# Kernel optimization log

Measured on AMD Instinct MI355X. Metric: run time of the kernel, lower is better.

The kernel has to match this reference:

```python
import jax, jax.numpy as jnp
import numpy as np

D_MODEL = 1024
NUM_HEADS = 16
HEAD_DIM = D_MODEL // NUM_HEADS  # used only for score scaling, as in the torch code


def setup_inputs() -> dict:
    key = jax.random.key(0)
    ks = jax.random.split(key, 8)
    B, S, D = 4, 2048, D_MODEL
    w_scale = 1.0 / np.sqrt(D)
    return {
        "x": jax.random.normal(ks[0], (B, S, D), dtype=jnp.float32),
        "Wq": jax.random.normal(ks[1], (D, D), dtype=jnp.float32) * w_scale,
        "bq": jnp.zeros((D,), dtype=jnp.float32),
        "Wk": jax.random.normal(ks[2], (D, D), dtype=jnp.float32) * w_scale,
        "bk": jnp.zeros((D,), dtype=jnp.float32),
        "Wv": jax.random.normal(ks[3], (D, D), dtype=jnp.float32) * w_scale,
        "bv": jnp.zeros((D,), dtype=jnp.float32),
        "temperature_scale": jnp.ones((1,), dtype=jnp.float32),
    }


def reference(x, Wq, bq, Wk, bk, Wv, bv, temperature_scale):
    # q, k, v: (B, S, D) -- no head split in the original module
    q = x @ Wq + bq
    k = x @ Wk + bk
    v = x @ Wv + bv
    scale = jnp.asarray(HEAD_DIM, x.dtype) ** 0.5
    # scores: (B, S, S)
    scores = jnp.einsum("bqd,bkd->bqk", q, k) / scale / temperature_scale[0]
    probs = jax.nn.softmax(scores, axis=-1)
    # per-row attention entropy (B, S, 1)
    entropy = -jnp.sum(probs * jnp.log(probs + 1e-8), axis=-1, keepdims=True)
    attention_output = jnp.einsum("bqk,bkd->bqd", probs, v)
    return attention_output, entropy.mean()
```

## Files before the change

kernel.cpp:

```cpp
#include <hip/hip_runtime.h>
#include <hip/hip_bf16.h>
#include <cstdint>
#include <cstddef>


typedef __attribute__((ext_vector_type(8))) short short8;
typedef __attribute__((ext_vector_type(4))) short short4v;
typedef __attribute__((ext_vector_type(4))) float f32x4;

#define GLOBAL_AS __attribute__((address_space(1)))
#define LDS_AS __attribute__((address_space(3)))

__device__ __forceinline__ void async_load16(const void* g, void* lds) {
  __builtin_amdgcn_global_load_lds((GLOBAL_AS void*)g, (LDS_AS void*)lds, 16, 0, 0);
}

__device__ __forceinline__ short f2bf_s(float x) {
  __hip_bfloat16 h = __float2bfloat16(x);
  return *reinterpret_cast<short*>(&h);
}

template <int MODE>
__device__ __forceinline__
void gemm_body(const __hip_bfloat16* __restrict__ A,
               const __hip_bfloat16* __restrict__ Bt,
               void* __restrict__ Cout,
               const float* __restrict__ bias,
               int K, int lda, int ldb, int ldc,
               __hip_bfloat16* __restrict__ sA,
               __hip_bfloat16* __restrict__ sB,
               int m0, int n0,
               const float* __restrict__ aux,
               float* __restrict__ stats) {
  const int tid  = threadIdx.x;
  const int lane = tid & 63;
  const int wid  = tid >> 6;
  const int wm = (wid >> 1) * 64;
  const int wn = (wid & 1) * 64;
  const int quad = lane >> 4;
  const int rc   = lane & 15;

  f32x4 acc[4][4] = {};

  const int srow = tid >> 3;
  const int scol = ((tid & 7) ^ ((tid >> 3) & 7)) * 8;
  const __hip_bfloat16* Ag = A  + (size_t)(m0 + srow) * lda + scol;
  const __hip_bfloat16* Bg = Bt + (size_t)(n0 + srow) * ldb + scol;

  for (int k0 = 0; k0 < K; k0 += 64) {
#pragma unroll
    for (int p = 0; p < 4; ++p) {
      async_load16(Ag + k0 + (size_t)(32 * p) * lda, &sA[(wid * 64 + 256 * p) * 8]);
      async_load16(Bg + k0 + (size_t)(32 * p) * ldb, &sB[(wid * 64 + 256 * p) * 8]);
    }
    __syncthreads();

#pragma unroll
    for (int kk = 0; kk < 2; ++kk) {
      const int xo = ((kk * 4 + quad) ^ (rc & 7)) * 8;
      short8 af[4], bf[4];
#pragma unroll
      for (int i = 0; i < 4; ++i)
        af[i] = *(const short8*)&sA[(wm + i * 16 + rc) * 64 + xo];
#pragma unroll
      for (int i = 0; i < 4; ++i)
        bf[i] = *(const short8*)&sB[(wn + i * 16 + rc) * 64 + xo];

#pragma unroll
      for (int mi = 0; mi < 4; ++mi)
#pragma unroll
        for (int ni = 0; ni < 4; ++ni)
          acc[mi][ni] = __builtin_amdgcn_mfma_f32_16x16x32_bf16(
              af[mi], bf[ni], acc[mi][ni], 0, 0, 0);
    }
    __syncthreads();
  }

  if (MODE == 3) {
    const int chunk = (n0 + wn) >> 6;
#pragma unroll
    for (int mi = 0; mi < 4; ++mi) {
      float l_acc[4] = {}, w_acc[4] = {};
#pragma unroll
      for (int ni = 0; ni < 4; ++ni)
#pragma unroll
        for (int r = 0; r < 4; ++r) {
          const float xv = acc[mi][ni][r];
          const float e = __expf(xv);
          acc[mi][ni][r] = e;
          l_acc[r] += e;
          w_acc[r] += e * xv;
        }
#pragma unroll
      for (int r = 0; r < 4; ++r) {
        float l = l_acc[r], w = w_acc[r];
#pragma unroll
        for (int off = 1; off < 16; off <<= 1) {
          l += __shfl_xor(l, off);
          w += __shfl_xor(w, off);
        }
        if (rc == 0) {
          const int row = m0 + wm + mi * 16 + quad * 4 + r;
          *(float2*)&stats[((size_t)row * 32 + chunk) * 2] = make_float2(l, w);
        }
      }
#pragma unroll
      for (int ni = 0; ni < 4; ++ni) {
        const int col = n0 + wn + ni * 16 + rc;
#pragma unroll
        for (int r = 0; r < 4; ++r) {
          const int row = m0 + wm + mi * 16 + quad * 4 + r;
          ((__hip_bfloat16*)Cout)[(size_t)row * ldc + col] =
              __float2bfloat16(acc[mi][ni][r]);
        }
      }
    }
  } else if (MODE == 4) {
    float* lred = (float*)sA;
    {
      const int row2 = tid >> 1;
      const float* sp = aux + (size_t)(m0 + row2) * 64 + (tid & 1) * 32;
      float l = 0.f, w = 0.f;
#pragma unroll
      for (int j = 0; j < 8; ++j) {
        const float4 a = *(const float4*)(sp + j * 4);
        l += a.x + a.z;
        w += a.y + a.w;
      }
      l += __shfl_xor(l, 1);
      w += __shfl_xor(w, 1);
      if ((tid & 1) == 0) {
        lred[row2] = 1.0f / l;
        if (stats) stats[m0 + row2] = __logf(l) - w / l;
      }
    }
    __syncthreads();
#pragma unroll
    for (int mi = 0; mi < 4; ++mi) {
      float sc[4];
#pragma unroll
      for (int r = 0; r < 4; ++r)
        sc[r] = lred[wm + mi * 16 + quad * 4 + r];
#pragma unroll
      for (int ni = 0; ni < 4; ++ni) {
        const int col = n0 + wn + ni * 16 + rc;
#pragma unroll
        for (int r = 0; r < 4; ++r) {
          const int row = m0 + wm + mi * 16 + quad * 4 + r;
          ((float*)Cout)[(size_t)row * ldc + col] = acc[mi][ni][r] * sc[r];
        }
      }
    }
  } else {
    const float qsc = (MODE == 1 && aux) ? 1.0f / (8.0f * aux[0]) : 1.0f;
#pragma unroll
    for (int mi = 0; mi < 4; ++mi) {
#pragma unroll
      for (int ni = 0; ni < 4; ++ni) {
        const int col = n0 + wn + ni * 16 + rc;
        const float badd = bias[col];
        if (MODE == 2) {
          const int rowb = m0 + wm + mi * 16 + quad * 4;
          short4v o;
#pragma unroll
          for (int r = 0; r < 4; ++r) o[r] = f2bf_s(acc[mi][ni][r] + badd);
          const size_t idx = (size_t)(rowb >> 11) * (1024u * 2048u) +
                             (size_t)col * 2048u + (size_t)(rowb & 2047);
          *(short4v*)((short*)Cout + idx) = o;
        } else {
#pragma unroll
          for (int r = 0; r < 4; ++r) {
            const int row = m0 + wm + mi * 16 + quad * 4 + r;
            ((__hip_bfloat16*)Cout)[(size_t)row * ldc + col] =
                __float2bfloat16((acc[mi][ni][r] + badd) * qsc);
          }
        }
      }
    }
  }
}


__global__ __launch_bounds__(256)
void qkv_fused(const __hip_bfloat16* __restrict__ xb,
               const __hip_bfloat16* __restrict__ Wt,
               __hip_bfloat16* __restrict__ qb, __hip_bfloat16* __restrict__ kb,
               __hip_bfloat16* __restrict__ vt,
               const float* __restrict__ bq, const float* __restrict__ bk,
               const float* __restrict__ bv, const float* __restrict__ tptr) {
  __shared__ __align__(16) __hip_bfloat16 sA[128 * 64];
  __shared__ __align__(16) __hip_bfloat16 sB[128 * 64];
  const int lin = blockIdx.x;
  const int j = lin & 7, t = lin >> 3;
  const int x = t & 7;
  const int G = j + 8 * (t >> 3);
  const int z = G >> 6, y = G & 63;
  const int m0 = y * 128, n0 = x * 128;

  const __hip_bfloat16* B = Wt + (size_t)z * 1024 * 1024;
  if (z == 0)
    gemm_body<1>(xb, B, qb, bq, 1024, 1024, 1024, 1024, sA, sB, m0, n0, tptr, nullptr);
  else if (z == 1)
    gemm_body<1>(xb, B, kb, bk, 1024, 1024, 1024, 1024, sA, sB, m0, n0, nullptr, nullptr);
  else
    gemm_body<2>(xb, B, vt, bv, 1024, 1024, 1024, 0, sA, sB, m0, n0, nullptr, nullptr);
}

__global__ __launch_bounds__(256)
void scores_swz(const __hip_bfloat16* __restrict__ qb,
                const __hip_bfloat16* __restrict__ kb,
                __hip_bfloat16* __restrict__ Pt,
                float* __restrict__ stats) {
  __shared__ __align__(16) __hip_bfloat16 sA[128 * 64];
  __shared__ __align__(16) __hip_bfloat16 sB[128 * 64];
  const int lin = blockIdx.x;
  const int j = lin & 7, t = lin >> 3;
  const int w = t & 15;
  const int G = j + 8 * (t >> 4);
  const size_t z = G >> 4;
  const int r = G & 15;
  const int y = (r >> 2) * 4 + (w >> 2);
  const int x = (r & 3) * 4 + (w & 3);
  gemm_body<3>(qb + z * 2048 * 1024, kb + z * 2048 * 1024,
               Pt + z * 2048 * 2048, nullptr, 1024, 1024, 1024, 2048,
               sA, sB, y * 128, x * 128, nullptr, stats + z * 2048 * 64);
}

__global__ __launch_bounds__(256)
void pv_swz(const __hip_bfloat16* __restrict__ Pt,
            const __hip_bfloat16* __restrict__ vt,
            float* __restrict__ out,
            const float* __restrict__ stats,
            float* __restrict__ Hrow) {
  __shared__ __align__(16) __hip_bfloat16 sA[128 * 64];
  __shared__ __align__(16) __hip_bfloat16 sB[128 * 64];
  const int lin = blockIdx.x;
  const int j = lin & 7, t = lin >> 3;
  const int w = t & 3;
  const int G = j + 8 * (t >> 2);
  const size_t z = G >> 5;
  const int r = G & 31;
  const int y = (r >> 2) * 2 + (w >> 1);
  const int x = (r & 3) * 2 + (w & 1);
  gemm_body<4>(Pt + z * 2048 * 2048, vt + z * 1024 * 2048,
               out + z * 2048 * 1024, nullptr, 2048, 2048, 2048, 1024,
               sA, sB, y * 128, x * 128,
               stats + z * 2048 * 64,
               (x == 0) ? (Hrow + z * 2048) : nullptr);
}

__global__ __launch_bounds__(256)
void prep_fused(const float* __restrict__ x, __hip_bfloat16* __restrict__ xb,
                const float* __restrict__ Wq, const float* __restrict__ Wk,
                const float* __restrict__ Wv, __hip_bfloat16* __restrict__ Wt) {
  if (blockIdx.x < 4096) {
    const int i = (blockIdx.x * 256 + threadIdx.x) * 8;
    const float4 a = *(const float4*)(x + i);
    const float4 b = *(const float4*)(x + i + 4);
    short8 o;
    o[0] = f2bf_s(a.x); o[1] = f2bf_s(a.y); o[2] = f2bf_s(a.z); o[3] = f2bf_s(a.w);
    o[4] = f2bf_s(b.x); o[5] = f2bf_s(b.y); o[6] = f2bf_s(b.z); o[7] = f2bf_s(b.w);
    *(short8*)((short*)xb + i) = o;
  } else {
    __shared__ float tile[64][65];
    const int b = blockIdx.x - 4096;
    const int z = b >> 8;
    const int rem = b & 255;
    const int c0 = (rem & 15) * 64;
    const int r0 = (rem >> 4) * 64;
    const float* src = (z == 0) ? Wq : (z == 1) ? Wk : Wv;
    __hip_bfloat16* dst = Wt + (size_t)z * 1024 * 1024;
    const int lane = threadIdx.x & 63;
    const int grp  = threadIdx.x >> 6;
#pragma unroll
    for (int i = 0; i < 16; ++i) {
      const int r = grp * 16 + i;
      tile[r][lane] = src[(size_t)(r0 + r) * 1024 + c0 + lane];
    }
    __syncthreads();
#pragma unroll
    for (int i = 0; i < 16; ++i) {
      const int r = grp * 16 + i;
      dst[(size_t)(c0 + r) * 1024 + r0 + lane] = __float2bfloat16(tile[lane][r]);
    }
  }
}

__global__ __launch_bounds__(256)
void reduce_entropy(const float* __restrict__ Hrow, float* __restrict__ out) {
  const int tid  = threadIdx.x;
  const int lane = tid & 63;
  const int wid  = tid >> 6;
  float s = 0.f;
#pragma unroll
  for (int j = 0; j < 8; ++j) {
    const float4 a = *(const float4*)(Hrow + j * 1024 + tid * 4);
    s += a.x + a.y + a.z + a.w;
  }
#pragma unroll
  for (int off = 1; off < 64; off <<= 1) s += __shfl_xor(s, off);
  __shared__ float red[4];
  if (lane == 0) red[wid] = s;
  __syncthreads();
  if (tid == 0)
    out[0] = (red[0] + red[1] + red[2] + red[3]) * (1.0f / 8192.0f);
}

extern "C" void kernel_launch(void* const* d_in, const int* in_sizes, int n_in,
                              void* d_out, int out_size, void* d_ws, size_t ws_size,
                              hipStream_t stream) {
  const float* x    = (const float*)d_in[0];
  const float* Wq   = (const float*)d_in[1];
  const float* bq   = (const float*)d_in[2];
  const float* Wk   = (const float*)d_in[3];
  const float* bk   = (const float*)d_in[4];
  const float* Wv   = (const float*)d_in[5];
  const float* bv   = (const float*)d_in[6];
  const float* temp = (const float*)d_in[7];
  float* out = (float*)d_out;
  char* ws = (char*)d_ws;

  __hip_bfloat16* qb    = (__hip_bfloat16*)(ws + 0);
  __hip_bfloat16* kb    = (__hip_bfloat16*)(ws + 16777216);
  __hip_bfloat16* vt    = (__hip_bfloat16*)(ws + 33554432);
  __hip_bfloat16* xb    = (__hip_bfloat16*)(ws + 50331648);
  __hip_bfloat16* Wt    = (__hip_bfloat16*)(ws + 67108864);
  __hip_bfloat16* Pt    = (__hip_bfloat16*)(ws + 73400320);
  float*          stats = (float*)(ws + 106954752);
  float*          Hrow  = (float*)(ws + 109084672);

  prep_fused<<<4864, 256, 0, stream>>>(x, xb, Wq, Wk, Wv, Wt);

  qkv_fused<<<1536, 256, 0, stream>>>(xb, Wt, qb, kb, vt, bq, bk, bv, temp);

  scores_swz<<<1024, 256, 0, stream>>>(qb, kb, Pt, stats);
  pv_swz<<<512, 256, 0, stream>>>(Pt, vt, out, stats, Hrow);

  reduce_entropy<<<1, 256, 0, stream>>>(Hrow, out + 8388608);
}
```

Measured before the change: 252.0 us.

## Enlarge scores GEMM tile to 256x128 and hoist softmax stats reduction

The scores GEMM moves to a dedicated 512-thread kernel with 256x128 output tiles, so each K tile loaded into shared memory is reused by more rows. This cuts global and LDS load traffic per MFMA, at the cost of more shared memory per block and fewer blocks in flight. The per-row reduction of partial softmax sums and entropy terms, previously done inside every PV block, now runs once in a small separate kernel that writes inverse normalisers and row entropies. The PV epilogue then just reads the precomputed scale, which removes redundant work and one block-wide barrier but adds an extra kernel launch.

```diff
diff --git a/kernel.cpp b/kernel.cpp
--- a/kernel.cpp
+++ b/kernel.cpp
@@ -30,8 +30,7 @@
                __hip_bfloat16* __restrict__ sA,
                __hip_bfloat16* __restrict__ sB,
                int m0, int n0,
-               const float* __restrict__ aux,
-               float* __restrict__ stats) {
+               const float* __restrict__ aux) {
   const int tid  = threadIdx.x;
   const int lane = tid & 63;
   const int wid  = tid >> 6;
@@ -76,71 +75,13 @@
     __syncthreads();
   }
 
-  if (MODE == 3) {
-    const int chunk = (n0 + wn) >> 6;
-#pragma unroll
-    for (int mi = 0; mi < 4; ++mi) {
-      float l_acc[4] = {}, w_acc[4] = {};
-#pragma unroll
-      for (int ni = 0; ni < 4; ++ni)
-#pragma unroll
-        for (int r = 0; r < 4; ++r) {
-          const float xv = acc[mi][ni][r];
-          const float e = __expf(xv);
-          acc[mi][ni][r] = e;
-          l_acc[r] += e;
-          w_acc[r] += e * xv;
-        }
-#pragma unroll
-      for (int r = 0; r < 4; ++r) {
-        float l = l_acc[r], w = w_acc[r];
-#pragma unroll
-        for (int off = 1; off < 16; off <<= 1) {
-          l += __shfl_xor(l, off);
-          w += __shfl_xor(w, off);
-        }
-        if (rc == 0) {
-          const int row = m0 + wm + mi * 16 + quad * 4 + r;
-          *(float2*)&stats[((size_t)row * 32 + chunk) * 2] = make_float2(l, w);
-        }
-      }
-#pragma unroll
-      for (int ni = 0; ni < 4; ++ni) {
-        const int col = n0 + wn + ni * 16 + rc;
-#pragma unroll
-        for (int r = 0; r < 4; ++r) {
-          const int row = m0 + wm + mi * 16 + quad * 4 + r;
-          ((__hip_bfloat16*)Cout)[(size_t)row * ldc + col] =
-              __float2bfloat16(acc[mi][ni][r]);
-        }
-      }
-    }
-  } else if (MODE == 4) {
-    float* lred = (float*)sA;
-    {
-      const int row2 = tid >> 1;
-      const float* sp = aux + (size_t)(m0 + row2) * 64 + (tid & 1) * 32;
-      float l = 0.f, w = 0.f;
-#pragma unroll
-      for (int j = 0; j < 8; ++j) {
-        const float4 a = *(const float4*)(sp + j * 4);
-        l += a.x + a.z;
-        w += a.y + a.w;
-      }
-      l += __shfl_xor(l, 1);
-      w += __shfl_xor(w, 1);
-      if ((tid & 1) == 0) {
-        lred[row2] = 1.0f / l;
-        if (stats) stats[m0 + row2] = __logf(l) - w / l;
-      }
-    }
-    __syncthreads();
+  if (MODE == 4) {
 #pragma unroll
     for (int mi = 0; mi < 4; ++mi) {
       float sc[4];
 #pragma unroll
       for (int r = 0; r < 4; ++r)
-        sc[r] = lred[wm + mi * 16 + quad * 4 + r];
+        sc[r] = aux[m0 + wm + mi * 16 + quad * 4 + r];
 #pragma unroll
       for (int ni = 0; ni < 4; ++ni) {
         const int col = n0 + wn + ni * 16 + rc;
@@ -179,7 +120,6 @@
     }
   }
 }
-
 
 __global__ __launch_bounds__(256)
 void qkv_fused(const __hip_bfloat16* __restrict__ xb,
@@ -199,39 +139,121 @@
 
   const __hip_bfloat16* B = Wt + (size_t)z * 1024 * 1024;
   if (z == 0)
-    gemm_body<1>(xb, B, qb, bq, 1024, 1024, 1024, 1024, sA, sB, m0, n0, tptr, nullptr);
+    gemm_body<1>(xb, B, qb, bq, 1024, 1024, 1024, 1024, sA, sB, m0, n0, tptr);
   else if (z == 1)
-    gemm_body<1>(xb, B, kb, bk, 1024, 1024, 1024, 1024, sA, sB, m0, n0, nullptr, nullptr);
+    gemm_body<1>(xb, B, kb, bk, 1024, 1024, 1024, 1024, sA, sB, m0, n0, nullptr);
   else
-    gemm_body<2>(xb, B, vt, bv, 1024, 1024, 1024, 0, sA, sB, m0, n0, nullptr, nullptr);
-}
-
-__global__ __launch_bounds__(256)
-void scores_swz(const __hip_bfloat16* __restrict__ qb,
-                const __hip_bfloat16* __restrict__ kb,
-                __hip_bfloat16* __restrict__ Pt,
-                float* __restrict__ stats) {
-  __shared__ __align__(16) __hip_bfloat16 sA[128 * 64];
+    gemm_body<2>(xb, B, vt, bv, 1024, 1024, 1024, 0, sA, sB, m0, n0, nullptr);
+}
+
+__global__ __launch_bounds__(512)
+void scores_bigm(const __hip_bfloat16* __restrict__ qb,
+                 const __hip_bfloat16* __restrict__ kb,
+                 __hip_bfloat16* __restrict__ Pt,
+                 float* __restrict__ stats) {
+  __shared__ __align__(16) __hip_bfloat16 sA[256 * 64];
   __shared__ __align__(16) __hip_bfloat16 sB[128 * 64];
   const int lin = blockIdx.x;
-  const int j = lin & 7, t = lin >> 3;
-  const int w = t & 15;
-  const int G = j + 8 * (t >> 4);
-  const size_t z = G >> 4;
-  const int r = G & 15;
-  const int y = (r >> 2) * 4 + (w >> 2);
-  const int x = (r & 3) * 4 + (w & 3);
-  gemm_body<3>(qb + z * 2048 * 1024, kb + z * 2048 * 1024,
-               Pt + z * 2048 * 2048, nullptr, 1024, 1024, 1024, 2048,
-               sA, sB, y * 128, x * 128, nullptr, stats + z * 2048 * 64);
+  const int G = (lin & 7) * 64 + (lin >> 3);
+  const size_t z = G >> 7;
+  const int rr = G & 127;
+  const int y = rr >> 4;
+  const int x = rr & 15;
+  const int m0 = y * 256, n0 = x * 128;
+  const __hip_bfloat16* A  = qb + z * 2048 * 1024;
+  const __hip_bfloat16* Bt = kb + z * 2048 * 1024;
+  __hip_bfloat16* Cout = Pt + z * 2048 * 2048;
+  float* st = stats + z * 2048 * 64;
+
+  const int tid  = threadIdx.x;
+  const int lane = tid & 63;
+  const int wid  = tid >> 6;
+  const int wm   = (wid >> 1) * 64;
+  const int wn   = (wid & 1) * 64;
+  const int quad = lane >> 4;
+  const int rc   = lane & 15;
+
+  f32x4 acc[4][4] = {};
+
+  const int srow = tid >> 3;
+  const int scol = ((tid & 7) ^ ((tid >> 3) & 7)) * 8;
+  const __hip_bfloat16* Ag = A  + (size_t)(m0 + srow) * 1024 + scol;
+  const __hip_bfloat16* Bg = Bt + (size_t)(n0 + srow) * 1024 + scol;
+
+  for (int k0 = 0; k0 < 1024; k0 += 64) {
+#pragma unroll
+    for (int p = 0; p < 4; ++p)
+      async_load16(Ag + k0 + (size_t)(64 * p) * 1024, &sA[(tid + 512 * p) * 8]);
+#pragma unroll
+    for (int p = 0; p < 2; ++p)
+      async_load16(Bg + k0 + (size_t)(64 * p) * 1024, &sB[(tid + 512 * p) * 8]);
+    __syncthreads();
+
+#pragma unroll
+    for (int kk = 0; kk < 2; ++kk) {
+      const int xo = ((kk * 4 + quad) ^ (rc & 7)) * 8;
+      short8 af[4], bf[4];
+#pragma unroll
+      for (int i = 0; i < 4; ++i)
+        af[i] = *(const short8*)&sA[(wm + i * 16 + rc) * 64 + xo];
+#pragma unroll
+      for (int i = 0; i < 4; ++i)
+        bf[i] = *(const short8*)&sB[(wn + i * 16 + rc) * 64 + xo];
+
+#pragma unroll
+      for (int mi = 0; mi < 4; ++mi)
+#pragma unroll
+        for (int ni = 0; ni < 4; ++ni)
+          acc[mi][ni] = __builtin_amdgcn_mfma_f32_16x16x32_bf16(
+              af[mi], bf[ni], acc[mi][ni], 0, 0, 0);
+    }
+    __syncthreads();
+  }
+
+  const int chunk = (n0 + wn) >> 6;
+#pragma unroll
+  for (int mi = 0; mi < 4; ++mi) {
+    float l_acc[4] = {}, w_acc[4] = {};
+#pragma unroll
+    for (int ni = 0; ni < 4; ++ni)
+#pragma unroll
+      for (int r = 0; r < 4; ++r) {
+        const float xv = acc[mi][ni][r];
+        const float e = __expf(xv);
+        acc[mi][ni][r] = e;
+        l_acc[r] += e;
+        w_acc[r] += e * xv;
+      }
+#pragma unroll
+    for (int r = 0; r < 4; ++r) {
+      float l = l_acc[r], w = w_acc[r];
+#pragma unroll
+      for (int off = 1; off < 16; off <<= 1) {
+        l += __shfl_xor(l, off);
+        w += __shfl_xor(w, off);
+      }
+      if (rc == 0) {
+        const int row = m0 + wm + mi * 16 + quad * 4 + r;
+        *(float2*)&st[((size_t)row * 32 + chunk) * 2] = make_float2(l, w);
+      }
+    }
+#pragma unroll
+    for (int ni = 0; ni < 4; ++ni) {
+      const int col = n0 + wn + ni * 16 + rc;
+#pragma unroll
+      for (int r = 0; r < 4; ++r) {
+        const int row = m0 + wm + mi * 16 + quad * 4 + r;
+        Cout[(size_t)row * 2048 + col] = __float2bfloat16(acc[mi][ni][r]);
+      }
+    }
+  }
 }
 
 __global__ __launch_bounds__(256)
 void pv_swz(const __hip_bfloat16* __restrict__ Pt,
             const __hip_bfloat16* __restrict__ vt,
             float* __restrict__ out,
-            const float* __restrict__ stats,
-            float* __restrict__ Hrow) {
+            const float* __restrict__ inv_l) {
   __shared__ __align__(16) __hip_bfloat16 sA[128 * 64];
   __shared__ __align__(16) __hip_bfloat16 sB[128 * 64];
   const int lin = blockIdx.x;
@@ -244,9 +266,7 @@
   const int x = (r & 3) * 2 + (w & 1);
   gemm_body<4>(Pt + z * 2048 * 2048, vt + z * 1024 * 2048,
                out + z * 2048 * 1024, nullptr, 2048, 2048, 2048, 1024,
-               sA, sB, y * 128, x * 128,
-               stats + z * 2048 * 64,
-               (x == 0) ? (Hrow + z * 2048) : nullptr);
+               sA, sB, y * 128, x * 128, inv_l + z * 2048);
 }
 
 __global__ __launch_bounds__(256)
@@ -287,6 +307,23 @@
 }
 
 __global__ __launch_bounds__(256)
+void stats_reduce(const float* __restrict__ stats,
+                  float* __restrict__ inv_l, float* __restrict__ Hrow) {
+  const int row = blockIdx.x * 256 + threadIdx.x;
+  const float* sp = stats + (size_t)row * 64;
+  float l = 0.f, w = 0.f;
+#pragma unroll
+  for (int j = 0; j < 16; ++j) {
+    const float4 a = *(const float4*)(sp + j * 4);
+    l += a.x + a.z;
+    w += a.y + a.w;
+  }
+  const float il = 1.0f / l;
+  inv_l[row] = il;
+  Hrow[row] = __logf(l) - w * il;
+}
+
+__global__ __launch_bounds__(256)
 void reduce_entropy(const float* __restrict__ Hrow, float* __restrict__ out) {
   const int tid  = threadIdx.x;
   const int lane = tid & 63;
@@ -327,14 +364,16 @@
   __hip_bfloat16* Wt    = (__hip_bfloat16*)(ws + 67108864);
   __hip_bfloat16* Pt    = (__hip_bfloat16*)(ws + 73400320);
   float*          stats = (float*)(ws + 106954752);
+  float*          inv_l = (float*)(ws + 109051904);
   float*          Hrow  = (float*)(ws + 109084672);
 
   prep_fused<<<4864, 256, 0, stream>>>(x, xb, Wq, Wk, Wv, Wt);
 
   qkv_fused<<<1536, 256, 0, stream>>>(xb, Wt, qb, kb, vt, bq, bk, bv, temp);
 
-  scores_swz<<<1024, 256, 0, stream>>>(qb, kb, Pt, stats);
-  pv_swz<<<512, 256, 0, stream>>>(Pt, vt, out, stats, Hrow);
+  scores_bigm<<<512, 512, 0, stream>>>(qb, kb, Pt, stats);
+  stats_reduce<<<32, 256, 0, stream>>>(stats, inv_l, Hrow);
+  pv_swz<<<512, 256, 0, stream>>>(Pt, vt, out, inv_l);
 
   reduce_entropy<<<1, 256, 0, stream>>>(Hrow, out + 8388608);
 }
```

After: 242.1 us (median of 2 runs). -3.9%, faster.
